# Optimization experiments

Measured on AMD Instinct MI355X. Metric: run time of the kernel, lower is better.

## Reference

```python
import jax, jax.numpy as jnp
import numpy as np

N = 100_000        # nodes
E = 1_600_000      # edges (avg degree 16)
NODE_DIM = 64
HIDDEN = 64
OUT = 32


def _glorot(key, fan_in, fan_out):
    lim = np.sqrt(6.0 / (fan_in + fan_out)).astype(np.float32)
    return jax.random.uniform(key, (fan_in, fan_out), jnp.float32, -lim, lim)


def setup_inputs() -> dict:
    key = jax.random.key(0)
    ks = jax.random.split(key, 5)
    x = jax.random.normal(ks[0], (N, NODE_DIM), jnp.float32)
    edge_index = jax.random.randint(ks[1], (2, E), 0, N, dtype=jnp.int64)
    return {
        "x": x,
        "edge_index": edge_index,
        "W1": _glorot(ks[2], NODE_DIM, HIDDEN),
        "b1": jnp.zeros((HIDDEN,), jnp.float32),
        "Wmu": _glorot(ks[3], HIDDEN, OUT),
        "bmu": jnp.zeros((OUT,), jnp.float32),
        "Wlv": _glorot(ks[4], HIDDEN, OUT),
        "blv": jnp.zeros((OUT,), jnp.float32),
    }


def _gcn_conv(h, W, b, src, dst, norm, n):
    """PyG GCNConv: linear (no bias) -> normalized scatter-add -> + bias.
    src/dst/norm already include self-loops and deg^{-1/2} symmetric norm."""
    h = h @ W                                   # [n, out]
    msg = h[src] * norm[:, None]                # [E+N, out] gather
    out = jax.ops.segment_sum(msg, dst, num_segments=n)  # scatter-add
    return out + b


def reference(x, edge_index, W1, b1, Wmu, bmu, Wlv, blv):
    loops = jnp.arange(N, dtype=edge_index.dtype)
    src = jnp.concatenate([edge_index[0], loops])  # add self-loops
    dst = jnp.concatenate([edge_index[1], loops])
    # symmetric normalization: deg computed on target nodes (all weights 1)
    deg = jax.ops.segment_sum(jnp.ones_like(src, dtype=x.dtype), dst, num_segments=N)
    dinv = jax.lax.rsqrt(deg)                   # deg >= 1 due to self-loops
    norm = dinv[src] * dinv[dst]

    h = jax.nn.relu(_gcn_conv(x, W1, b1, src, dst, norm, N))
    mu = _gcn_conv(h, Wmu, bmu, src, dst, norm, N)
    logvar = _gcn_conv(h, Wlv, blv, src, dst, norm, N)
    return mu, logvar
```

## Files before the change

### kernel.cpp

```cpp
#include <hip/hip_runtime.h>
#include <hip/hip_fp16.h>


#define BKT_SHIFT 9
#define BKT_NODES 512
#define CHUNK 8192
#define STAGE_CAP 10240

typedef __attribute__((ext_vector_type(8))) _Float16 half8;
typedef __attribute__((ext_vector_type(4))) float float4v;
typedef __attribute__((ext_vector_type(4))) unsigned uint4v;

__device__ __forceinline__ int imin(int a, int b) { return a < b ? a : b; }
__device__ __forceinline__ int imax(int a, int b) { return a > b ? a : b; }
__device__ __forceinline__ unsigned h2u(__half2 v) {
  union { __half2 h; unsigned u; } c; c.h = v; return c.u;
}
__device__ __forceinline__ __half2 u2h(unsigned x) {
  union { unsigned u; __half2 h; } c; c.u = x; return c.h;
}

__global__ __launch_bounds__(256) void bucket_count(const int* __restrict__ dst,
                                                    int* __restrict__ cnt,
                                                    int E, int nbk, int nblk) {
  __shared__ int hist[2][256];
  const int t = threadIdx.x;
  const int h = (t >> 7) & 1;
  hist[0][t] = 0;
  hist[1][t] = 0;
  __syncthreads();
  const int base = blockIdx.x * CHUNK;
  const int end = imin(base + CHUNK, E);
  for (int e = base + t * 4; e < end; e += 1024) {
    if (e + 3 < end) {
      const int4 d4 = *(const int4*)(dst + e);
      atomicAdd(&hist[h][d4.x >> BKT_SHIFT], 1);
      atomicAdd(&hist[h][d4.y >> BKT_SHIFT], 1);
      atomicAdd(&hist[h][d4.z >> BKT_SHIFT], 1);
      atomicAdd(&hist[h][d4.w >> BKT_SHIFT], 1);
    } else {
      for (int k = e; k < end; ++k) atomicAdd(&hist[h][dst[k] >> BKT_SHIFT], 1);
    }
  }
  __syncthreads();
  if (t < nbk) cnt[t * nblk + blockIdx.x] = hist[0][t] + hist[1][t];
}

__global__ __launch_bounds__(256) void scan_rows(int* __restrict__ cnt,
                                                 int* __restrict__ rowsum,
                                                 int nbk, int nblk) {
  __shared__ int red[256];
  const int b = blockIdx.x;
  const int t = threadIdx.x;
  const int v = (t < nblk) ? cnt[b * nblk + t] : 0;
  red[t] = v;
  __syncthreads();
  for (int off = 1; off < 256; off <<= 1) {
    const int u = (t >= off) ? red[t - off] : 0;
    __syncthreads();
    red[t] += u;
    __syncthreads();
  }
  if (t < nblk) cnt[b * nblk + t] = red[t] - v;
  if (t == 255) rowsum[b] = red[255];
}

__global__ __launch_bounds__(512) void bucket_scatter(const int* __restrict__ src,
                                                      const int* __restrict__ dst,
                                                      const int* __restrict__ cnt,
                                                      const int* __restrict__ rowsum,
                                                      int* __restrict__ tmp,
                                                      int E, int nbk, int nblk) {
  __shared__ int hist[2][256];
  __shared__ int lofs[256];
  __shared__ int gofs[256];
  __shared__ int cur[256];
  __shared__ int red[256];
  __shared__ int stage[CHUNK];
  const int t = threadIdx.x;
  const int c = blockIdx.x;
  hist[t >> 8][t & 255] = 0;
  __syncthreads();
  const int h = (t >> 8) & 1;
  const int base = c * CHUNK;
  const int end = imin(base + CHUNK, E);
  for (int e = base + t * 4; e < end; e += 2048) {
    if (e + 3 < end) {
      const int4 d4 = *(const int4*)(dst + e);
      atomicAdd(&hist[h][d4.x >> BKT_SHIFT], 1);
      atomicAdd(&hist[h][d4.y >> BKT_SHIFT], 1);
      atomicAdd(&hist[h][d4.z >> BKT_SHIFT], 1);
      atomicAdd(&hist[h][d4.w >> BKT_SHIFT], 1);
    } else {
      for (int k = e; k < end; ++k) atomicAdd(&hist[h][dst[k] >> BKT_SHIFT], 1);
    }
  }
  __syncthreads();
  int tot = 0;
  if (t < 256) {
    tot = hist[0][t] + hist[1][t];
    red[t] = tot;
  }
  __syncthreads();
  for (int off = 1; off < 256; off <<= 1) {
    int u = 0;
    if (t < 256 && t >= off) u = red[t - off];
    __syncthreads();
    if (t < 256) red[t] += u;
    __syncthreads();
  }
  if (t < 256) {
    lofs[t] = red[t] - tot;
    cur[t] = red[t] - tot;
  }
  __syncthreads();
  int rv = 0;
  if (t < 256) {
    rv = (t < nbk) ? rowsum[t] : 0;
    red[t] = rv;
  }
  __syncthreads();
  for (int off = 1; off < 256; off <<= 1) {
    int u = 0;
    if (t < 256 && t >= off) u = red[t - off];
    __syncthreads();
    if (t < 256) red[t] += u;
    __syncthreads();
  }
  if (t < nbk) gofs[t] = (red[t] - rv) + cnt[t * nblk + c];
  __syncthreads();
  for (int e = base + t * 4; e < end; e += 2048) {
    if (e + 3 < end) {
      const int4 s4 = *(const int4*)(src + e);
      const int4 d4 = *(const int4*)(dst + e);
      int p0 = atomicAdd(&cur[d4.x >> BKT_SHIFT], 1);
      stage[p0] = (s4.x << 9) | (d4.x & 511);
      int p1 = atomicAdd(&cur[d4.y >> BKT_SHIFT], 1);
      stage[p1] = (s4.y << 9) | (d4.y & 511);
      int p2 = atomicAdd(&cur[d4.z >> BKT_SHIFT], 1);
      stage[p2] = (s4.z << 9) | (d4.z & 511);
      int p3 = atomicAdd(&cur[d4.w >> BKT_SHIFT], 1);
      stage[p3] = (s4.w << 9) | (d4.w & 511);
    } else {
      for (int k = e; k < end; ++k) {
        const int d = dst[k];
        const int pos = atomicAdd(&cur[d >> BKT_SHIFT], 1);
        stage[pos] = (src[k] << 9) | (d & 511);
      }
    }
  }
  __syncthreads();
  const int wv = t >> 6, lane = t & 63;
  for (int b = wv; b < nbk; b += 8) {
    const int len = hist[0][b] + hist[1][b];
    const int lo = lofs[b];
    const int go = gofs[b];
    for (int k = lane; k < len; k += 64) tmp[go + k] = stage[lo + k];
  }
}

__global__ __launch_bounds__(1024) void bucket_build(const int* __restrict__ tmp,
                                                     const int* __restrict__ rowsum,
                                                     int* __restrict__ row_ptr,
                                                     int* __restrict__ pairs,
                                                     const float* __restrict__ x,
                                                     __half* __restrict__ xs,
                                                     __half* __restrict__ hs,
                                                     int n, int nbk, int E) {
  __shared__ int hist[BKT_NODES];
  __shared__ int scn[BKT_NODES];
  __shared__ int red[256];
  __shared__ int stage[STAGE_CAP];
  __shared__ int s_sh;
  const int b = blockIdx.x;
  const int t = threadIdx.x;
  const int node0 = b << BKT_SHIFT;
  int v0 = 0;
  if (t < 256) {
    v0 = (t < nbk) ? rowsum[t] : 0;
    red[t] = v0;
  }
  if (t < BKT_NODES) hist[t] = 0;
  __syncthreads();
  for (int off = 1; off < 256; off <<= 1) {
    int u = 0;
    if (t < 256 && t >= off) u = red[t - off];
    __syncthreads();
    if (t < 256) red[t] += u;
    __syncthreads();
  }
  if (t == 0) s_sh = red[b] - rowsum[b];
  __syncthreads();
  const int s = s_sh;
  const int e = s + rowsum[b];
  const int len = e - s;
  for (int k = s + t; k < e; k += 1024) atomicAdd(&hist[tmp[k] & 511], 1);
  __syncthreads();
  int v = 0;
  if (t < BKT_NODES) {
    v = hist[t];
    scn[t] = v;
  }
  __syncthreads();
  for (int off = 1; off < BKT_NODES; off <<= 1) {
    int u = 0;
    if (t < BKT_NODES && t >= off) u = scn[t - off];
    __syncthreads();
    if (t < BKT_NODES) scn[t] += u;
    __syncthreads();
  }
  const bool staged = (len <= STAGE_CAP);
  if (t < BKT_NODES) {
    const int lexcl = scn[t] - v;
    const int node = node0 + t;
    if (node < n) row_ptr[node] = s + lexcl;
    if (b == nbk - 1 && t == 0) row_ptr[n] = E;
    hist[t] = staged ? lexcl : (s + lexcl);
    scn[t] = __float_as_int(rsqrtf(1.0f + (float)v));
  }
  __syncthreads();
  if (staged) {
    for (int k = s + t; k < e; k += 1024) {
      const int w = tmp[k];
      const int pos = atomicAdd(&hist[w & 511], 1);
      stage[pos] = w >> 9;
    }
    __syncthreads();
    for (int k = t; k < len; k += 1024) pairs[s + k] = stage[k];
  } else {
    for (int k = s + t; k < e; k += 1024) {
      const int w = tmp[k];
      const int pos = atomicAdd(&hist[w & 511], 1);
      pairs[pos] = w >> 9;
    }
  }
  const int nloc = imin(BKT_NODES, n - node0);
  for (int idx = t; idx < nloc * 16; idx += 1024) {
    const int nl = idx >> 4, f4 = idx & 15;
    const float4 v4 = ((const float4*)x)[(size_t)(node0 + nl) * 16 + f4];
    const float d = __int_as_float(scn[nl]);
    __half2* o = (__half2*)(xs + (size_t)(node0 + nl) * 64 + f4 * 4);
    o[0] = __floats2half2_rn(d * v4.x, d * v4.y);
    o[1] = __floats2half2_rn(d * v4.z, d * v4.w);
  }
  if (b == 0 && t < 32) {
    if (t < 16)
      ((float2*)(xs + (size_t)n * 64))[t] = make_float2(0.f, 0.f);
    else
      ((float2*)(hs + (size_t)n * 64))[t - 16] = make_float2(0.f, 0.f);
  }
}


#define YSTRIDE 264

__global__ __launch_bounds__(256, 4) void agg_layer1(const __half* __restrict__ xs,
                                                     const int* __restrict__ pairs,
                                                     const int* __restrict__ row_ptr,
                                                     const float* __restrict__ W1,
                                                     const float* __restrict__ b1,
                                                     __half* __restrict__ hs, int n) {
  __shared__ _Float16 ylds_all[4][16 * YSTRIDE];
  __shared__ float dilds_all[4][16];
  const int wv = threadIdx.x >> 6;
  _Float16* ylds = ylds_all[wv];
  float* dilds = dilds_all[wv];
  const int lane = threadIdx.x & 63;
  const int g = lane >> 3, q = lane & 7;
  const int quad = lane >> 4, col = lane & 15;

  half8 bfrag[2][4];
#pragma unroll
  for (int s = 0; s < 2; ++s)
#pragma unroll
    for (int t = 0; t < 4; ++t)
#pragma unroll
      for (int jj = 0; jj < 8; ++jj)
        bfrag[s][t][jj] = (_Float16)W1[(s * 32 + quad * 8 + jj) * 64 + t * 16 + col];
  float bias[4];
#pragma unroll
  for (int t = 0; t < 4; ++t) bias[t] = b1[t * 16 + col];

  const int ntiles = (n + 15) >> 4;
  for (int tile = blockIdx.x * 4 + wv; tile < ntiles; tile += gridDim.x * 4) {
    const int row0 = tile << 4;
#pragma unroll 1
    for (int rg = 0; rg < 4; ++rg) {
      int start[4], end[4], idx[4];
      __half2 acc[4][4];
      int maxdeg = 0;
#pragma unroll
      for (int j = 0; j < 4; ++j) {
        const int i = row0 + rg * 4 + j;
        start[j] = 0; end[j] = 0;
        if (i < n) { start[j] = row_ptr[i]; end[j] = row_ptr[i + 1]; }
        maxdeg = imax(maxdeg, end[j] - start[j]);
#pragma unroll
        for (int k = 0; k < 4; ++k) acc[j][k] = u2h(0u);
        idx[j] = (start[j] + g < end[j]) ? pairs[start[j] + g] : n;
      }
      const int iters = (maxdeg + 7) >> 3;
#pragma unroll 1
      for (int it = 0; it < iters; ++it) {
        int nidx[4];
#pragma unroll
        for (int j = 0; j < 4; ++j) {
          const int ofs2 = start[j] + (it + 1) * 8 + g;
          nidx[j] = (ofs2 < end[j]) ? pairs[ofs2] : n;
        }
#pragma unroll
        for (int j = 0; j < 4; ++j) {
          const float4 rr = *(const float4*)(xs + (size_t)idx[j] * 64 + q * 8);
          const __half2* hp = (const __half2*)&rr;
#pragma unroll
          for (int k = 0; k < 4; ++k) acc[j][k] = __hadd2(acc[j][k], hp[k]);
        }
#pragma unroll
        for (int j = 0; j < 4; ++j) idx[j] = nidx[j];
      }
#pragma unroll
      for (int j = 0; j < 4; ++j) {
        const int i = row0 + rg * 4 + j;
        if (g == 0 && i < n) {
          const float4 sr = *(const float4*)(xs + (size_t)i * 64 + q * 8);
          const __half2* hp = (const __half2*)&sr;
#pragma unroll
          for (int k = 0; k < 4; ++k) acc[j][k] = __hadd2(acc[j][k], hp[k]);
        }
#pragma unroll
        for (int k = 0; k < 4; ++k) {
          unsigned u = __shfl_xor(h2u(acc[j][k]), 32);
          acc[j][k] = __hadd2(acc[j][k], u2h(u));
        }
        const float di = rsqrtf((float)(1 + end[j] - start[j]));
        const __half hdi = __float2half(di);
        const __half2 di2 = __halves2half2(hdi, hdi);
        uint4v st;
        st.x = h2u(__hmul2(di2, acc[j][0]));
        st.y = h2u(__hmul2(di2, acc[j][1]));
        st.z = h2u(__hmul2(di2, acc[j][2]));
        st.w = h2u(__hmul2(di2, acc[j][3]));
        *(uint4v*)(ylds + (rg * 4 + j) * YSTRIDE + (g & 3) * 64 + q * 8) = st;
        if (lane == 0) dilds[rg * 4 + j] = di;
      }
    }
    float4v acc[4];
#pragma unroll
    for (int t = 0; t < 4; ++t) acc[t] = (float4v){bias[t], bias[t], bias[t], bias[t]};
#pragma unroll
    for (int s2 = 0; s2 < 8; ++s2) {
      half8 af = *(half8*)(ylds + col * YSTRIDE + s2 * 32 + quad * 8);
      const int sW = s2 & 1;
#pragma unroll
      for (int t = 0; t < 4; ++t)
        acc[t] = __builtin_amdgcn_mfma_f32_16x16x32_f16(af, bfrag[sW][t], acc[t], 0, 0, 0);
    }
    const float4 dis = *(const float4*)(dilds + quad * 4);
    const float dd[4] = {dis.x, dis.y, dis.z, dis.w};
#pragma unroll
    for (int t = 0; t < 4; ++t)
#pragma unroll
      for (int reg = 0; reg < 4; ++reg) {
        const int row = row0 + quad * 4 + reg;
        if (row < n)
          hs[(size_t)row * 64 + t * 16 + col] =
              __float2half(dd[reg] * fmaxf(acc[t][reg], 0.f));
      }
  }
}

__global__ __launch_bounds__(256, 4) void agg_layer2(const __half* __restrict__ hsin,
                                                     const int* __restrict__ pairs,
                                                     const int* __restrict__ row_ptr,
                                                     const float* __restrict__ Wmu,
                                                     const float* __restrict__ bmu,
                                                     const float* __restrict__ Wlv,
                                                     const float* __restrict__ blv,
                                                     float* __restrict__ out_mu,
                                                     float* __restrict__ out_lv, int n) {
  __shared__ _Float16 ylds_all[4][16 * YSTRIDE];
  const int wv = threadIdx.x >> 6;
  _Float16* ylds = ylds_all[wv];
  const int lane = threadIdx.x & 63;
  const int g = lane >> 3, q = lane & 7;
  const int quad = lane >> 4, col = lane & 15;

  half8 bfrag[2][4];
#pragma unroll
  for (int s = 0; s < 2; ++s)
#pragma unroll
    for (int t = 0; t < 4; ++t) {
      const int j = t * 16 + col;
      const float* W = (j < 32) ? Wmu : Wlv;
      const int jc = j & 31;
#pragma unroll
      for (int jj = 0; jj < 8; ++jj)
        bfrag[s][t][jj] = (_Float16)W[(s * 32 + quad * 8 + jj) * 32 + jc];
    }
  float bias[4];
#pragma unroll
  for (int t = 0; t < 4; ++t) {
    const int j = t * 16 + col;
    bias[t] = (j < 32) ? bmu[j] : blv[j - 32];
  }

  const int ntiles = (n + 15) >> 4;
  for (int tile = blockIdx.x * 4 + wv; tile < ntiles; tile += gridDim.x * 4) {
    const int row0 = tile << 4;
#pragma unroll 1
    for (int rg = 0; rg < 4; ++rg) {
      int start[4], end[4], idx[4];
      __half2 acc[4][4];
      int maxdeg = 0;
#pragma unroll
      for (int j = 0; j < 4; ++j) {
        const int i = row0 + rg * 4 + j;
        start[j] = 0; end[j] = 0;
        if (i < n) { start[j] = row_ptr[i]; end[j] = row_ptr[i + 1]; }
        maxdeg = imax(maxdeg, end[j] - start[j]);
#pragma unroll
        for (int k = 0; k < 4; ++k) acc[j][k] = u2h(0u);
        idx[j] = (start[j] + g < end[j]) ? pairs[start[j] + g] : n;
      }
      const int iters = (maxdeg + 7) >> 3;
#pragma unroll 1
      for (int it = 0; it < iters; ++it) {
        int nidx[4];
#pragma unroll
        for (int j = 0; j < 4; ++j) {
          const int ofs2 = start[j] + (it + 1) * 8 + g;
          nidx[j] = (ofs2 < end[j]) ? pairs[ofs2] : n;
        }
#pragma unroll
        for (int j = 0; j < 4; ++j) {
          const float4 rr = *(const float4*)(hsin + (size_t)idx[j] * 64 + q * 8);
          const __half2* hp = (const __half2*)&rr;
#pragma unroll
          for (int k = 0; k < 4; ++k) acc[j][k] = __hadd2(acc[j][k], hp[k]);
        }
#pragma unroll
        for (int j = 0; j < 4; ++j) idx[j] = nidx[j];
      }
#pragma unroll
      for (int j = 0; j < 4; ++j) {
        const int i = row0 + rg * 4 + j;
        if (g == 0 && i < n) {
          const float4 sr = *(const float4*)(hsin + (size_t)i * 64 + q * 8);
          const __half2* hp = (const __half2*)&sr;
#pragma unroll
          for (int k = 0; k < 4; ++k) acc[j][k] = __hadd2(acc[j][k], hp[k]);
        }
#pragma unroll
        for (int k = 0; k < 4; ++k) {
          unsigned u = __shfl_xor(h2u(acc[j][k]), 32);
          acc[j][k] = __hadd2(acc[j][k], u2h(u));
        }
        const float di = rsqrtf((float)(1 + end[j] - start[j]));
        const __half hdi = __float2half(di);
        const __half2 di2 = __halves2half2(hdi, hdi);
        uint4v st;
        st.x = h2u(__hmul2(di2, acc[j][0]));
        st.y = h2u(__hmul2(di2, acc[j][1]));
        st.z = h2u(__hmul2(di2, acc[j][2]));
        st.w = h2u(__hmul2(di2, acc[j][3]));
        *(uint4v*)(ylds + (rg * 4 + j) * YSTRIDE + (g & 3) * 64 + q * 8) = st;
      }
    }
    float4v acc[4];
#pragma unroll
    for (int t = 0; t < 4; ++t) acc[t] = (float4v){bias[t], bias[t], bias[t], bias[t]};
#pragma unroll
    for (int s2 = 0; s2 < 8; ++s2) {
      half8 af = *(half8*)(ylds + col * YSTRIDE + s2 * 32 + quad * 8);
      const int sW = s2 & 1;
#pragma unroll
      for (int t = 0; t < 4; ++t)
        acc[t] = __builtin_amdgcn_mfma_f32_16x16x32_f16(af, bfrag[sW][t], acc[t], 0, 0, 0);
    }
#pragma unroll
    for (int t = 0; t < 4; ++t)
#pragma unroll
      for (int reg = 0; reg < 4; ++reg) {
        const int row = row0 + quad * 4 + reg;
        if (row < n) {
          const int j = t * 16 + col;
          if (j < 32)
            out_mu[(size_t)row * 32 + j] = acc[t][reg];
          else
            out_lv[(size_t)row * 32 + (j - 32)] = acc[t][reg];
        }
      }
  }
}

extern "C" void kernel_launch(void* const* d_in, const int* in_sizes, int n_in,
                              void* d_out, int out_size, void* d_ws, size_t ws_size,
                              hipStream_t stream) {
  const float* x = (const float*)d_in[0];
  const int* ei = (const int*)d_in[1];
  const float* W1 = (const float*)d_in[2];
  const float* b1 = (const float*)d_in[3];
  const float* Wmu = (const float*)d_in[4];
  const float* bmu = (const float*)d_in[5];
  const float* Wlv = (const float*)d_in[6];
  const float* blv = (const float*)d_in[7];

  const int N = in_sizes[0] / 64;
  const int E = in_sizes[1] / 2;
  const int* src = ei;
  const int* dst = ei + E;

  const int NBK = (N + BKT_NODES - 1) >> BKT_SHIFT;
  const int NBLK = (E + CHUNK - 1) / CHUNK;
  const int FL = NBK * NBLK;

  auto align256 = [](size_t v) { return (v + 255) & ~(size_t)255; };
  char* p = (char*)d_ws;
  int* row_ptr = (int*)p;  p += align256((size_t)(N + 1) * 4);
  int* rowsum = (int*)p;   p += align256((size_t)256 * 4);
  int* cnt = (int*)p;      p += align256((size_t)FL * 4);
  int* pairs = (int*)p;    p += align256((size_t)E * 4);
  __half* xs = (__half*)p; p += align256((size_t)(N + 1) * 64 * 2);
  size_t tmp_bytes = (size_t)E * 4;
  size_t hs_bytes = (size_t)(N + 1) * 64 * 2;
  int* tmp = (int*)p;
  __half* hs = (__half*)p;
  p += align256(tmp_bytes > hs_bytes ? tmp_bytes : hs_bytes);

  float* out_mu = (float*)d_out;
  float* out_lv = out_mu + (size_t)N * 32;

  bucket_count<<<NBLK, 256, 0, stream>>>(dst, cnt, E, NBK, NBLK);
  scan_rows<<<NBK, 256, 0, stream>>>(cnt, rowsum, NBK, NBLK);
  bucket_scatter<<<NBLK, 512, 0, stream>>>(src, dst, cnt, rowsum, tmp, E, NBK, NBLK);
  bucket_build<<<NBK, 1024, 0, stream>>>(tmp, rowsum, row_ptr, pairs, x, xs, hs,
                                         N, NBK, E);

  const int ntiles = (N + 15) / 16;
  const int ablocks = (ntiles + 3) / 4;
  agg_layer1<<<ablocks, 256, 0, stream>>>(xs, pairs, row_ptr, W1, b1, hs, N);
  agg_layer2<<<ablocks, 256, 0, stream>>>(hs, pairs, row_ptr, Wmu, bmu, Wlv, blv,
                                          out_mu, out_lv, N);
}
```

Measured before the change: 229.6 us.

## Split feature cast out of bucket_build and halve edge chunk size

Moves the dinv-scaled fp32→fp16 cast of x out of the bucket_build kernel, which launches only one block per 512-node bucket, into a separate elementwise kernel that covers the whole grid. dinv is now written to a new workspace buffer for that purpose. The edge chunk size is halved so the count and scatter stages launch twice as many blocks, with bucket_count widened to 512 threads. scan_rows now handles two entries per thread so it still covers the larger block count. This adds one kernel launch and an extra global round trip for dinv in exchange for better parallelism in the preprocessing stages.

```diff
diff --git a/kernel.cpp b/kernel.cpp
--- a/kernel.cpp
+++ b/kernel.cpp
@@ -4,7 +4,7 @@
 
 #define BKT_SHIFT 9
 #define BKT_NODES 512
-#define CHUNK 8192
+#define CHUNK 4096
 #define STAGE_CAP 10240
 
 typedef __attribute__((ext_vector_type(8))) _Float16 half8;
@@ -20,18 +20,17 @@
   union { unsigned u; __half2 h; } c; c.u = x; return c.h;
 }
 
-__global__ __launch_bounds__(256) void bucket_count(const int* __restrict__ dst,
+__global__ __launch_bounds__(512) void bucket_count(const int* __restrict__ dst,
                                                     int* __restrict__ cnt,
                                                     int E, int nbk, int nblk) {
   __shared__ int hist[2][256];
   const int t = threadIdx.x;
-  const int h = (t >> 7) & 1;
-  hist[0][t] = 0;
-  hist[1][t] = 0;
-  __syncthreads();
+  hist[t >> 8][t & 255] = 0;
+  __syncthreads();
+  const int h = (t >> 8) & 1;
   const int base = blockIdx.x * CHUNK;
   const int end = imin(base + CHUNK, E);
-  for (int e = base + t * 4; e < end; e += 1024) {
+  for (int e = base + t * 4; e < end; e += 2048) {
     if (e + 3 < end) {
       const int4 d4 = *(const int4*)(dst + e);
       atomicAdd(&hist[h][d4.x >> BKT_SHIFT], 1);
@@ -52,8 +51,12 @@
   __shared__ int red[256];
   const int b = blockIdx.x;
   const int t = threadIdx.x;
-  const int v = (t < nblk) ? cnt[b * nblk + t] : 0;
-  red[t] = v;
+  const int rbase = b * nblk;
+  const int i0 = 2 * t, i1 = 2 * t + 1;
+  const int v0 = (i0 < nblk) ? cnt[rbase + i0] : 0;
+  const int v1 = (i1 < nblk) ? cnt[rbase + i1] : 0;
+  const int run = v0 + v1;
+  red[t] = run;
   __syncthreads();
   for (int off = 1; off < 256; off <<= 1) {
     const int u = (t >= off) ? red[t - off] : 0;
@@ -61,8 +64,10 @@
     red[t] += u;
     __syncthreads();
   }
-  if (t < nblk) cnt[b * nblk + t] = red[t] - v;
+  const int acc = red[t] - run;
   if (t == 255) rowsum[b] = red[255];
+  if (i0 < nblk) cnt[rbase + i0] = acc;
+  if (i1 < nblk) cnt[rbase + i1] = acc + v0;
 }
 
 __global__ __launch_bounds__(512) void bucket_scatter(const int* __restrict__ src,
@@ -162,10 +167,8 @@
 __global__ __launch_bounds__(1024) void bucket_build(const int* __restrict__ tmp,
                                                      const int* __restrict__ rowsum,
                                                      int* __restrict__ row_ptr,
+                                                     float* __restrict__ dinv,
                                                      int* __restrict__ pairs,
-                                                     const float* __restrict__ x,
-                                                     __half* __restrict__ xs,
-                                                     __half* __restrict__ hs,
                                                      int n, int nbk, int E) {
   __shared__ int hist[BKT_NODES];
   __shared__ int scn[BKT_NODES];
@@ -213,10 +216,12 @@
   if (t < BKT_NODES) {
     const int lexcl = scn[t] - v;
     const int node = node0 + t;
-    if (node < n) row_ptr[node] = s + lexcl;
+    if (node < n) {
+      row_ptr[node] = s + lexcl;
+      dinv[node] = rsqrtf(1.0f + (float)v);
+    }
     if (b == nbk - 1 && t == 0) row_ptr[n] = E;
     hist[t] = staged ? lexcl : (s + lexcl);
-    scn[t] = __float_as_int(rsqrtf(1.0f + (float)v));
   }
   __syncthreads();
   if (staged) {
@@ -234,20 +239,26 @@
       pairs[pos] = w >> 9;
     }
   }
-  const int nloc = imin(BKT_NODES, n - node0);
-  for (int idx = t; idx < nloc * 16; idx += 1024) {
-    const int nl = idx >> 4, f4 = idx & 15;
-    const float4 v4 = ((const float4*)x)[(size_t)(node0 + nl) * 16 + f4];
-    const float d = __int_as_float(scn[nl]);
-    __half2* o = (__half2*)(xs + (size_t)(node0 + nl) * 64 + f4 * 4);
-    o[0] = __floats2half2_rn(d * v4.x, d * v4.y);
-    o[1] = __floats2half2_rn(d * v4.z, d * v4.w);
-  }
-  if (b == 0 && t < 32) {
-    if (t < 16)
-      ((float2*)(xs + (size_t)n * 64))[t] = make_float2(0.f, 0.f);
+}
+
+__global__ __launch_bounds__(256) void cast_scale(const float* __restrict__ x,
+                                                  const float* __restrict__ dinv,
+                                                  __half* __restrict__ xs,
+                                                  __half* __restrict__ hs,
+                                                  int n4, int nrow) {
+  int i = blockIdx.x * blockDim.x + threadIdx.x;
+  if (i < n4) {
+    float4 v = ((const float4*)x)[i];
+    float d = dinv[i >> 4];
+    __half2* o = (__half2*)(xs + (size_t)i * 4);
+    o[0] = __floats2half2_rn(d * v.x, d * v.y);
+    o[1] = __floats2half2_rn(d * v.z, d * v.w);
+  } else if (i < n4 + 32) {
+    int j = i - n4;
+    if (j < 16)
+      ((float2*)(xs + (size_t)nrow * 64))[j] = make_float2(0.f, 0.f);
     else
-      ((float2*)(hs + (size_t)n * 64))[t - 16] = make_float2(0.f, 0.f);
+      ((float2*)(hs + (size_t)nrow * 64))[j - 16] = make_float2(0.f, 0.f);
   }
 }
 
@@ -517,6 +528,7 @@
   auto align256 = [](size_t v) { return (v + 255) & ~(size_t)255; };
   char* p = (char*)d_ws;
   int* row_ptr = (int*)p;  p += align256((size_t)(N + 1) * 4);
+  float* dinv = (float*)p; p += align256((size_t)N * 4);
   int* rowsum = (int*)p;   p += align256((size_t)256 * 4);
   int* cnt = (int*)p;      p += align256((size_t)FL * 4);
   int* pairs = (int*)p;    p += align256((size_t)E * 4);
@@ -530,11 +542,14 @@
   float* out_mu = (float*)d_out;
   float* out_lv = out_mu + (size_t)N * 32;
 
-  bucket_count<<<NBLK, 256, 0, stream>>>(dst, cnt, E, NBK, NBLK);
+  const int n4 = N * 16;
+
+  bucket_count<<<NBLK, 512, 0, stream>>>(dst, cnt, E, NBK, NBLK);
   scan_rows<<<NBK, 256, 0, stream>>>(cnt, rowsum, NBK, NBLK);
   bucket_scatter<<<NBLK, 512, 0, stream>>>(src, dst, cnt, rowsum, tmp, E, NBK, NBLK);
-  bucket_build<<<NBK, 1024, 0, stream>>>(tmp, rowsum, row_ptr, pairs, x, xs, hs,
-                                         N, NBK, E);
+  bucket_build<<<NBK, 1024, 0, stream>>>(tmp, rowsum, row_ptr, dinv, pairs, N, NBK, E);
+
+  cast_scale<<<(n4 + 32 + 255) / 256, 256, 0, stream>>>(x, dinv, xs, hs, n4, N);
 
   const int ntiles = (N + 15) / 16;
   const int ablocks = (ntiles + 3) / 4;
```

Result: faster. 224.4 us (-2.2%).
